# Performance work log

Measured on AMD Instinct MI355X. Metric: run time of the kernel, lower is better.

The kernel has to match this reference:

```python
import jax, jax.numpy as jnp
import numpy as np

N = 100000   # nodes
E = 1200000  # edges
C = 64       # in_channels
H = 64       # hidden_channels
OUT = 10     # out_channels
G = 128      # graphs in batch
L = 3        # num_conv_layers
EPS = 1e-5   # BatchNorm eps


def batchnorm(x, g, b):
    # training-mode BatchNorm1d: biased batch stats over the node/graph axis
    mu = x.mean(axis=0)
    var = x.var(axis=0)
    return (x - mu) * jax.lax.rsqrt(var + EPS) * g + b


def _gcn_norm(edge_index):
    # add self-loops (weight 1) then symmetric normalization deg^-1/2 * w * deg^-1/2
    loop = jnp.arange(N)
    src = jnp.concatenate([edge_index[0], loop])
    dst = jnp.concatenate([edge_index[1], loop])
    w = jnp.ones((E + N,), jnp.float32)
    deg = jax.ops.segment_sum(w, src, num_segments=N)
    dis = jnp.where(deg > 0, jax.lax.rsqrt(deg), 0.0)
    norm = dis[src] * w * dis[dst]
    return src, dst, norm


def gcn_conv(h, W, b, src, dst, norm):
    # linear transform -> gather source features -> edge-normalize -> scatter-add to dst
    hw = h @ W
    msg = norm[:, None] * hw[src]          # [E+N, H]
    return jax.ops.segment_sum(msg, dst, num_segments=N) + b


def setup_inputs() -> dict:
    key = jax.random.key(0)
    ks = jax.random.split(key, 8)
    s = 0.1
    return {
        'x': jax.random.normal(ks[0], (N, C), jnp.float32),
        'edge_index': jax.random.randint(ks[1], (2, E), 0, N),
        'batch_idx': jnp.sort(jax.random.randint(ks[2], (N,), 0, G)),
        # BN params initialized as in the module: weight=1, bias=1e-4
        'bn_feat_g': jnp.ones((C,), jnp.float32),
        'bn_feat_b': jnp.full((C,), 1e-4, jnp.float32),
        'W_feat': jax.random.normal(ks[3], (C, H), jnp.float32) * s,  # conv_feat (gfn=True -> pure linear)
        'b_feat': jnp.zeros((H,), jnp.float32),
        'conv_bn_g': jnp.ones((L, H), jnp.float32),
        'conv_bn_b': jnp.full((L, H), 1e-4, jnp.float32),
        'conv_W': jax.random.normal(ks[4], (L, H, H), jnp.float32) * s,
        'conv_b': jnp.zeros((L, H), jnp.float32),
        'bn_fc_g': jnp.ones((H,), jnp.float32),
        'bn_fc_b': jnp.full((H,), 1e-4, jnp.float32),
        'W_fc': jax.random.normal(ks[5], (H, H), jnp.float32) * s,
        'b_fc': jnp.zeros((H,), jnp.float32),
        'bn_hid_g': jnp.ones((H,), jnp.float32),
        'bn_hid_b': jnp.full((H,), 1e-4, jnp.float32),
        'W_cls': jax.random.normal(ks[6], (H, OUT), jnp.float32) * s,
        'b_cls': jnp.zeros((OUT,), jnp.float32),
    }


def reference(x, edge_index, batch_idx, bn_feat_g, bn_feat_b, W_feat, b_feat,
              conv_bn_g, conv_bn_b, conv_W, conv_b, bn_fc_g, bn_fc_b, W_fc, b_fc,
              bn_hid_g, bn_hid_b, W_cls, b_cls):
    src, dst, norm = _gcn_norm(edge_index)
    # forward_BNConvReLU, residual=False, gating=None, xg=None, dropout=0
    h = batchnorm(x, bn_feat_g, bn_feat_b)
    h = jax.nn.relu(h @ W_feat + b_feat)           # conv_feat: gfn=True => linear only
    for i in range(L):
        h_ = batchnorm(h, conv_bn_g[i], conv_bn_b[i])
        h = jax.nn.relu(gcn_conv(h_, conv_W[i], conv_b[i], src, dst, norm))
    hg = jax.ops.segment_sum(h, batch_idx, num_segments=G)  # global_add_pool -> [G, H]
    h_ = batchnorm(hg, bn_fc_g, bn_fc_b)
    hg = jax.nn.relu(h_ @ W_fc + b_fc)
    hg = batchnorm(hg, bn_hid_g, bn_hid_b)
    logits = hg @ W_cls + b_cls
    return jax.nn.log_softmax(logits, axis=-1)
```

## Files before the change

### kernel.cpp

```cpp
#include <hip/hip_runtime.h>
#include <hip/hip_fp16.h>

#define N_NODES 100000
#define N_EDGES 1200000
#define GRAPHS 128
#define EPSBN 1e-5f


__global__ __launch_bounds__(256) void k_build(const int* __restrict__ src,
                                               const int* __restrict__ dst,
                                               int* __restrict__ cnt,
                                               int* __restrict__ deg,
                                               int* __restrict__ ecsr) {
    int e = blockIdx.x * 256 + threadIdx.x;
    if (e < N_EDGES) {
        int s = src[e], d = dst[e];
        atomicAdd(&deg[s], 1);
        int p = atomicAdd(&cnt[d], 1);
        ecsr[(d << 6) + p] = s;
    }
}

__global__ __launch_bounds__(256) void k_dis(const int* __restrict__ deg,
                                             float* __restrict__ dis) {
    int i = blockIdx.x * 256 + threadIdx.x;
    if (i < N_NODES) dis[i] = rsqrtf((float)deg[i] + 1.0f);
}


__global__ __launch_bounds__(256) void k_sigma(const float* __restrict__ dis,
                                               const int* __restrict__ cnt,
                                               const int* __restrict__ ecsr,
                                               float* __restrict__ sigma) {
    int lane = threadIdx.x & 63;
    int wid = threadIdx.x >> 6;
    for (int node = blockIdx.x * 4 + wid; node < N_NODES; node += gridDim.x * 4) {
        int m = cnt[node];
        float v = 0.f;
        if (lane < m) v = dis[ecsr[(node << 6) + lane]];
#pragma unroll
        for (int d = 1; d <= 32; d <<= 1) v += __shfl_xor(v, d, 64);
        if (lane == 0) {
            float dd = dis[node];
            sigma[node] = dd * (v + dd);
        }
    }
}


__global__ __launch_bounds__(256) void k_stats(const float* __restrict__ x,
                                               float* __restrict__ sums) {
    const float4* x4 = (const float4*)x;
    int t = threadIdx.x;
    int q = t & 15, rg = t >> 4;
    float4 s = {0.f, 0.f, 0.f, 0.f}, s2 = {0.f, 0.f, 0.f, 0.f};
    for (int r = blockIdx.x * 16 + rg; r < N_NODES; r += gridDim.x * 16) {
        float4 v = x4[r * 16 + q];
        s.x += v.x; s.y += v.y; s.z += v.z; s.w += v.w;
        s2.x += v.x * v.x; s2.y += v.y * v.y; s2.z += v.z * v.z; s2.w += v.w * v.w;
    }
    __shared__ float red[2][16][64];
    red[0][rg][q * 4 + 0] = s.x;  red[0][rg][q * 4 + 1] = s.y;
    red[0][rg][q * 4 + 2] = s.z;  red[0][rg][q * 4 + 3] = s.w;
    red[1][rg][q * 4 + 0] = s2.x; red[1][rg][q * 4 + 1] = s2.y;
    red[1][rg][q * 4 + 2] = s2.z; red[1][rg][q * 4 + 3] = s2.w;
    __syncthreads();
    if (t < 64) {
        float a = 0.f, b = 0.f;
#pragma unroll
        for (int k = 0; k < 16; k++) { a += red[0][k][t]; b += red[1][k][t]; }
        atomicAdd(&sums[t], a);
        atomicAdd(&sums[64 + t], b);
    }
}


__global__ __launch_bounds__(256) void k_fold(const float* __restrict__ sums, const float* __restrict__ g,
                       const float* __restrict__ b, const float* __restrict__ W,
                       const float* __restrict__ bias_in, int has_bias,
                       float* __restrict__ Wout, float* __restrict__ bout) {
    __shared__ float a[64], cc[64];
    int t = threadIdx.x;
    if (t < 64) {
        float mu = sums[t] * (1.0f / N_NODES);
        float var = sums[64 + t] * (1.0f / N_NODES) - mu * mu;
        float av = g[t] * rsqrtf(var + EPSBN);
        a[t] = av;
        cc[t] = b[t] - mu * av;
    }
    __syncthreads();
    for (int i = t; i < 4096; i += 256) Wout[i] = a[i >> 6] * W[i];
    if (t < 64) {
        float acc = has_bias ? bias_in[t] : 0.0f;
        for (int k = 0; k < 64; k++) acc += cc[k] * W[k * 64 + t];
        bout[t] = acc;
    }
}


__global__ __launch_bounds__(256, 4) void k_gemm2(const float* __restrict__ X, const float* __restrict__ W,
                        const float* __restrict__ bias, const float* __restrict__ dis,
                        __half* __restrict__ U,
                        float* __restrict__ sums, int do_stats) {
    int t = threadIdx.x;
    int j = t & 63;
    int rg = t >> 6;
    __shared__ float wlds[64][64];
    __shared__ float xs[16][64];
    for (int i = t; i < 4096; i += 256) wlds[i >> 6][i & 63] = W[i];
    float bj = bias[j];
    __syncthreads();
    float s_sum = 0.f, s_sq = 0.f;
    for (int base = blockIdx.x * 16; base < N_NODES; base += gridDim.x * 16) {
        ((float4*)xs)[t] = ((const float4*)(X + base * 64))[t];
        int r0 = rg * 4;
        float a0 = bj, a1 = bj, a2 = bj, a3 = bj;
#pragma unroll
        for (int c = 0; c < 64; c++) {
            float w = wlds[c][j];
            a0 += xs[r0 + 0][c] * w;
            a1 += xs[r0 + 1][c] * w;
            a2 += xs[r0 + 2][c] * w;
            a3 += xs[r0 + 3][c] * w;
        }
        a0 = fmaxf(a0, 0.f); a1 = fmaxf(a1, 0.f);
        a2 = fmaxf(a2, 0.f); a3 = fmaxf(a3, 0.f);
        int nb = base + r0;
        U[(nb + 0) * 64 + j] = __float2half_rn(a0 * dis[nb + 0]);
        U[(nb + 1) * 64 + j] = __float2half_rn(a1 * dis[nb + 1]);
        U[(nb + 2) * 64 + j] = __float2half_rn(a2 * dis[nb + 2]);
        U[(nb + 3) * 64 + j] = __float2half_rn(a3 * dis[nb + 3]);
        if (do_stats) {
            s_sum += a0 + a1 + a2 + a3;
            s_sq += a0 * a0 + a1 * a1 + a2 * a2 + a3 * a3;
        }
    }
    if (do_stats) {
        __syncthreads();
        xs[rg][j] = s_sum;
        xs[4 + rg][j] = s_sq;
        __syncthreads();
        if (t < 64) {
            atomicAdd(&sums[t], xs[0][t] + xs[1][t] + xs[2][t] + xs[3][t]);
            atomicAdd(&sums[64 + t], xs[4][t] + xs[5][t] + xs[6][t] + xs[7][t]);
        }
    }
}


__global__ __launch_bounds__(256, 4) void k_aggemm(const __half* __restrict__ u,
                        const float* __restrict__ dis, const float* __restrict__ sigma,
                        const int* __restrict__ cnt, const int* __restrict__ ecsr,
                        const float* __restrict__ sums_in, const float* __restrict__ bng,
                        const float* __restrict__ bnb,
                        const float* __restrict__ W, const float* __restrict__ bias,
                        __half* __restrict__ uout, float* __restrict__ hout, int last,
                        float* __restrict__ sums_out, int do_stats) {
    const __half2* u2 = (const __half2*)u;
    int t = threadIdx.x;
    int j = t & 63;
    int wid = t >> 6;
    int g = j >> 5, c = j & 31;
    __shared__ float wlds[64][64];
    __shared__ float xs[16][64];
    if (t < 64) {
        float mu = sums_in[t] * (1.0f / N_NODES);
        float var = sums_in[64 + t] * (1.0f / N_NODES) - mu * mu;
        float av = bng[t] * rsqrtf(var + EPSBN);
        xs[0][t] = av;
        xs[1][t] = bnb[t] - mu * av;
    }
    __syncthreads();
    for (int i = t; i < 4096; i += 256) wlds[i >> 6][i & 63] = W[i] * xs[0][i >> 6];
    float cb = 0.f;
#pragma unroll 8
    for (int q = 0; q < 64; q++) cb += xs[1][q] * W[q * 64 + j];
    float bj = bias[j];
    __syncthreads();
    float s_sum = 0.f, s_sq = 0.f;
    for (int base = blockIdx.x * 16; base < N_NODES; base += gridDim.x * 16) {
        int r0 = wid * 4;
        float dvals[4], svals[4];
        for (int r = 0; r < 4; r++) {
            int node = base + r0 + r;
            int m = cnt[node];
            dvals[r] = dis[node];
            svals[r] = sigma[node];
            int sL = 0;
            if (j < m) sL = ecsr[(node << 6) + j];
            float ax = 0.f, ay = 0.f;
#pragma unroll
            for (int k = 0; k < 8; k++) {
                int e = 2 * k + g;
                int sE = __shfl(sL, e, 64);
                float w = (e < m) ? 1.0f : 0.0f;
                float2 f = __half22float2(u2[sE * 32 + c]);
                ax += w * f.x; ay += w * f.y;
            }
            if (m > 16) {
                for (int e = 16 + g; e < m; e += 2) {
                    int sE = __shfl(sL, e, 64);
                    float2 f = __half22float2(u2[sE * 32 + c]);
                    ax += f.x; ay += f.y;
                }
            }
            ax += __shfl_xor(ax, 32, 64);
            ay += __shfl_xor(ay, 32, 64);
            if (g == 0) {
                float2 sf = __half22float2(u2[node * 32 + c]);
                float dd = dvals[r];
                xs[r0 + r][2 * c + 0] = dd * (ax + sf.x);
                xs[r0 + r][2 * c + 1] = dd * (ay + sf.y);
            }
        }
        float a0 = bj + svals[0] * cb, a1 = bj + svals[1] * cb;
        float a2 = bj + svals[2] * cb, a3 = bj + svals[3] * cb;
#pragma unroll
        for (int q = 0; q < 64; q++) {
            float w = wlds[q][j];
            a0 += xs[r0 + 0][q] * w;
            a1 += xs[r0 + 1][q] * w;
            a2 += xs[r0 + 2][q] * w;
            a3 += xs[r0 + 3][q] * w;
        }
        a0 = fmaxf(a0, 0.f); a1 = fmaxf(a1, 0.f);
        a2 = fmaxf(a2, 0.f); a3 = fmaxf(a3, 0.f);
        int nb = base + r0;
        if (last) {
            hout[(nb + 0) * 64 + j] = a0;
            hout[(nb + 1) * 64 + j] = a1;
            hout[(nb + 2) * 64 + j] = a2;
            hout[(nb + 3) * 64 + j] = a3;
        } else {
            uout[(nb + 0) * 64 + j] = __float2half_rn(a0 * dvals[0]);
            uout[(nb + 1) * 64 + j] = __float2half_rn(a1 * dvals[1]);
            uout[(nb + 2) * 64 + j] = __float2half_rn(a2 * dvals[2]);
            uout[(nb + 3) * 64 + j] = __float2half_rn(a3 * dvals[3]);
        }
        if (do_stats) {
            s_sum += a0 + a1 + a2 + a3;
            s_sq += a0 * a0 + a1 * a1 + a2 * a2 + a3 * a3;
        }
    }
    if (do_stats) {
        __syncthreads();
        xs[wid][j] = s_sum;
        xs[4 + wid][j] = s_sq;
        __syncthreads();
        if (t < 64) {
            atomicAdd(&sums_out[t], xs[0][t] + xs[1][t] + xs[2][t] + xs[3][t]);
            atomicAdd(&sums_out[64 + t], xs[4][t] + xs[5][t] + xs[6][t] + xs[7][t]);
        }
    }
}


__global__ __launch_bounds__(256) void k_pool(const float* __restrict__ h, const int* __restrict__ batch,
                       float* __restrict__ hg, float* __restrict__ sums) {
    int g = blockIdx.x;
    int lo = 0, hi = N_NODES;
    while (lo < hi) { int m = (lo + hi) >> 1; if (batch[m] < g) lo = m + 1; else hi = m; }
    int start = lo;
    lo = start; hi = N_NODES;
    while (lo < hi) { int m = (lo + hi) >> 1; if (batch[m] < g + 1) lo = m + 1; else hi = m; }
    int end = lo;
    int c = threadIdx.x & 63, rg = threadIdx.x >> 6;
    float s = 0.f;
    for (int r = start + rg; r < end; r += 4) s += h[r * 64 + c];
    __shared__ float ls[4][64];
    ls[rg][c] = s;
    __syncthreads();
    if (rg == 0) {
        float v = ls[0][c] + ls[1][c] + ls[2][c] + ls[3][c];
        hg[g * 64 + c] = v;
        atomicAdd(&sums[c], v);
        atomicAdd(&sums[64 + c], v * v);
    }
}


__global__ __launch_bounds__(512) void k_tail(const float* __restrict__ hg_in, const float* __restrict__ sums,
                       const float* __restrict__ g1, const float* __restrict__ b1,
                       const float* __restrict__ Wfc, const float* __restrict__ bfc,
                       const float* __restrict__ g2, const float* __restrict__ b2,
                       const float* __restrict__ Wcls, const float* __restrict__ bcls,
                       float* __restrict__ out) {
    __shared__ float hgn[8192];
    __shared__ float h2[8192];
    __shared__ float red[2][8][64];
    __shared__ float a[64], cc[64];
    __shared__ float Wc[640];
    __shared__ float logits[1280];
    __shared__ float lse[128];
    int t = threadIdx.x;
    int j = t & 63;
    int w = t >> 6;

    if (t < 64) {
        float mu = sums[t] * (1.f / 128.f);
        float var = sums[64 + t] * (1.f / 128.f) - mu * mu;
        float av = g1[t] * rsqrtf(var + EPSBN);
        a[t] = av; cc[t] = b1[t] - mu * av;
    }
    for (int i = t; i < 640; i += 512) Wc[i] = Wcls[i];
    __syncthreads();
    for (int i = t; i < 8192; i += 512) hgn[i] = hg_in[i] * a[i & 63] + cc[i & 63];

    float wreg[64];
#pragma unroll
    for (int q = 0; q < 64; q++) wreg[q] = Wfc[q * 64 + j];
    float bj = bfc[j];
    __syncthreads();

    float acc[16];
#pragma unroll
    for (int r = 0; r < 16; r++) acc[r] = bj;
    const float4* hgn4 = (const float4*)hgn;
#pragma unroll
    for (int q4 = 0; q4 < 16; q4++) {
#pragma unroll
        for (int r = 0; r < 16; r++) {
            float4 hv = hgn4[(w * 16 + r) * 16 + q4];
            acc[r] += hv.x * wreg[q4 * 4 + 0] + hv.y * wreg[q4 * 4 + 1]
                    + hv.z * wreg[q4 * 4 + 2] + hv.w * wreg[q4 * 4 + 3];
        }
    }
    float s = 0.f, s2 = 0.f;
#pragma unroll
    for (int r = 0; r < 16; r++) {
        float v = fmaxf(acc[r], 0.f);
        h2[(w * 16 + r) * 64 + j] = v;
        s += v; s2 += v * v;
    }
    red[0][w][j] = s; red[1][w][j] = s2;
    __syncthreads();

    if (t < 64) {
        float su = 0.f, sq = 0.f;
#pragma unroll
        for (int k = 0; k < 8; k++) { su += red[0][k][t]; sq += red[1][k][t]; }
        float mu = su * (1.f / 128.f);
        float var = sq * (1.f / 128.f) - mu * mu;
        float av = g2[t] * rsqrtf(var + EPSBN);
        a[t] = av; cc[t] = b2[t] - mu * av;
    }
    __syncthreads();
    for (int i = t; i < 8192; i += 512) h2[i] = h2[i] * a[i & 63] + cc[i & 63];
    __syncthreads();

    for (int idx = t; idx < 1280; idx += 512) {
        int row = idx / 10, o = idx - row * 10;
        float v = bcls[o];
#pragma unroll
        for (int q = 0; q < 64; q++) v += h2[row * 64 + q] * Wc[q * 10 + o];
        logits[idx] = v;
    }
    __syncthreads();
    if (t < 128) {
        float mx = -1e30f;
#pragma unroll
        for (int o = 0; o < 10; o++) mx = fmaxf(mx, logits[t * 10 + o]);
        float se = 0.f;
#pragma unroll
        for (int o = 0; o < 10; o++) se += expf(logits[t * 10 + o] - mx);
        lse[t] = mx + logf(se);
    }
    __syncthreads();
    for (int idx = t; idx < 1280; idx += 512) out[idx] = logits[idx] - lse[idx / 10];
}


extern "C" void kernel_launch(void* const* d_in, const int* in_sizes, int n_in,
                              void* d_out, int out_size, void* d_ws, size_t ws_size,
                              hipStream_t stream) {
    const float* x         = (const float*)d_in[0];
    const int*   ei        = (const int*)  d_in[1];
    const int*   batch     = (const int*)  d_in[2];
    const float* bn_feat_g = (const float*)d_in[3];
    const float* bn_feat_b = (const float*)d_in[4];
    const float* W_feat    = (const float*)d_in[5];
    const float* b_feat    = (const float*)d_in[6];
    const float* conv_bn_g = (const float*)d_in[7];
    const float* conv_bn_b = (const float*)d_in[8];
    const float* conv_W    = (const float*)d_in[9];
    const float* conv_b    = (const float*)d_in[10];
    const float* bn_fc_g   = (const float*)d_in[11];
    const float* bn_fc_b   = (const float*)d_in[12];
    const float* W_fc      = (const float*)d_in[13];
    const float* b_fc      = (const float*)d_in[14];
    const float* bn_hid_g  = (const float*)d_in[15];
    const float* bn_hid_b  = (const float*)d_in[16];
    const float* W_cls     = (const float*)d_in[17];
    const float* b_cls     = (const float*)d_in[18];
    float* out = (float*)d_out;

    float* ws    = (float*)d_ws;
    float* hbuf  = ws;
    __half* u_a  = (__half*)(ws + 6400000);
    __half* u_b  = (__half*)(ws + 9600000);
    float* dis   = ws + 12800000;
    float* sigma = ws + 12900000;
    float* Wt    = ws + 13000000;
    float* bt    = Wt + 4096;
    float* hg    = bt + 64;
    float* sums  = hg + 8192;
    int*   cnt   = (int*)(sums + 640);
    int*   ecsr  = cnt + 100000;
    int*   deg   = (int*)u_b;

    float* sx = sums;
    float* s0 = sums + 128;
    float* s1 = sums + 256;
    float* s2 = sums + 384;
    float* s3 = sums + 512;

    const int* srcp = ei;
    const int* dstp = ei + N_EDGES;

    hipMemsetAsync(sums, 0, (640 + 100000) * sizeof(float), stream);
    hipMemsetAsync(deg, 0, 100000 * sizeof(int), stream);

    k_build<<<(N_EDGES + 255) / 256, 256, 0, stream>>>(srcp, dstp, cnt, deg, ecsr);
    k_dis<<<(N_NODES + 255) / 256, 256, 0, stream>>>(deg, dis);
    k_sigma<<<1024, 256, 0, stream>>>(dis, cnt, ecsr, sigma);

    k_stats<<<512, 256, 0, stream>>>(x, sx);
    k_fold<<<1, 256, 0, stream>>>(sx, bn_feat_g, bn_feat_b, W_feat, b_feat, 1, Wt, bt);
    k_gemm2<<<2048, 256, 0, stream>>>(x, Wt, bt, dis, u_a, s0, 1);

    k_aggemm<<<2048, 256, 0, stream>>>(u_a, dis, sigma, cnt, ecsr,
                                       s0, conv_bn_g + 0, conv_bn_b + 0,
                                       conv_W + 0, conv_b + 0,
                                       u_b, nullptr, 0, s1, 1);
    k_aggemm<<<2048, 256, 0, stream>>>(u_b, dis, sigma, cnt, ecsr,
                                       s1, conv_bn_g + 64, conv_bn_b + 64,
                                       conv_W + 4096, conv_b + 64,
                                       u_a, nullptr, 0, s2, 1);
    k_aggemm<<<2048, 256, 0, stream>>>(u_a, dis, sigma, cnt, ecsr,
                                       s2, conv_bn_g + 128, conv_bn_b + 128,
                                       conv_W + 8192, conv_b + 128,
                                       nullptr, hbuf, 1, nullptr, 0);

    k_pool<<<GRAPHS, 256, 0, stream>>>(hbuf, batch, hg, s3);
    k_tail<<<1, 512, 0, stream>>>(hg, s3, bn_fc_g, bn_fc_b, W_fc, b_fc,
                                  bn_hid_g, bn_hid_b, W_cls, b_cls, out);
}
```

Before: 629.0 us.

## Split pooling across more blocks, vectorize LDS matmuls, hoist per-node loads

Global pooling now runs four blocks per graph that each atomically add a quarter-range partial into a zeroed hg buffer. The graph-level BN statistics move into the tail kernel. The LDS matmul inner loops in k_gemm2 and k_aggemm now read float4 rows, and k_aggemm loads the per-node cnt/ecsr/dis/sigma/self features for all four rows up front to expose memory-level parallelism. k_sigma issues its loads unconditionally. Extra register pressure and atomics on hg are the trade-offs.

```diff
diff --git a/kernel.cpp b/kernel.cpp
--- a/kernel.cpp
+++ b/kernel.cpp
@@ -36,14 +36,13 @@
     int wid = threadIdx.x >> 6;
     for (int node = blockIdx.x * 4 + wid; node < N_NODES; node += gridDim.x * 4) {
         int m = cnt[node];
-        float v = 0.f;
-        if (lane < m) v = dis[ecsr[(node << 6) + lane]];
+        int sraw = ecsr[(node << 6) + lane];
+        float dd = dis[node];
+        int sL = (lane < m) ? sraw : 0;
+        float v = (lane < m) ? dis[sL] : 0.f;
 #pragma unroll
         for (int d = 1; d <= 32; d <<= 1) v += __shfl_xor(v, d, 64);
-        if (lane == 0) {
-            float dd = dis[node];
-            sigma[node] = dd * (v + dd);
-        }
+        if (lane == 0) sigma[node] = dd * (v + dd);
     }
 }
 
@@ -115,13 +114,18 @@
         ((float4*)xs)[t] = ((const float4*)(X + base * 64))[t];
         int r0 = rg * 4;
         float a0 = bj, a1 = bj, a2 = bj, a3 = bj;
-#pragma unroll
-        for (int c = 0; c < 64; c++) {
-            float w = wlds[c][j];
-            a0 += xs[r0 + 0][c] * w;
-            a1 += xs[r0 + 1][c] * w;
-            a2 += xs[r0 + 2][c] * w;
-            a3 += xs[r0 + 3][c] * w;
+        const float4* x0 = (const float4*)xs[r0 + 0];
+        const float4* x1 = (const float4*)xs[r0 + 1];
+        const float4* x2 = (const float4*)xs[r0 + 2];
+        const float4* x3 = (const float4*)xs[r0 + 3];
+#pragma unroll
+        for (int q4 = 0; q4 < 16; q4++) {
+            float w0 = wlds[q4 * 4 + 0][j], w1 = wlds[q4 * 4 + 1][j];
+            float w2 = wlds[q4 * 4 + 2][j], w3 = wlds[q4 * 4 + 3][j];
+            float4 v0 = x0[q4]; a0 += v0.x * w0 + v0.y * w1 + v0.z * w2 + v0.w * w3;
+            float4 v1 = x1[q4]; a1 += v1.x * w0 + v1.y * w1 + v1.z * w2 + v1.w * w3;
+            float4 v2 = x2[q4]; a2 += v2.x * w0 + v2.y * w1 + v2.z * w2 + v2.w * w3;
+            float4 v3 = x3[q4]; a3 += v3.x * w0 + v3.y * w1 + v3.z * w2 + v3.w * w3;
         }
         a0 = fmaxf(a0, 0.f); a1 = fmaxf(a1, 0.f);
         a2 = fmaxf(a2, 0.f); a3 = fmaxf(a3, 0.f);
@@ -180,14 +184,22 @@
     float s_sum = 0.f, s_sq = 0.f;
     for (int base = blockIdx.x * 16; base < N_NODES; base += gridDim.x * 16) {
         int r0 = wid * 4;
+        int nb = base + r0;
+        int mm[4], srw[4];
         float dvals[4], svals[4];
+        __half2 selfs[4];
+#pragma unroll
         for (int r = 0; r < 4; r++) {
-            int node = base + r0 + r;
-            int m = cnt[node];
-            dvals[r] = dis[node];
-            svals[r] = sigma[node];
-            int sL = 0;
-            if (j < m) sL = ecsr[(node << 6) + j];
+            mm[r] = cnt[nb + r];
+            srw[r] = ecsr[((nb + r) << 6) + j];
+            dvals[r] = dis[nb + r];
+            svals[r] = sigma[nb + r];
+            selfs[r] = u2[(nb + r) * 32 + c];
+        }
+#pragma unroll
+        for (int r = 0; r < 4; r++) {
+            int m = mm[r];
+            int sL = (j < m) ? srw[r] : 0;
             float ax = 0.f, ay = 0.f;
 #pragma unroll
             for (int k = 0; k < 8; k++) {
@@ -207,7 +219,7 @@
             ax += __shfl_xor(ax, 32, 64);
             ay += __shfl_xor(ay, 32, 64);
             if (g == 0) {
-                float2 sf = __half22float2(u2[node * 32 + c]);
+                float2 sf = __half22float2(selfs[r]);
                 float dd = dvals[r];
                 xs[r0 + r][2 * c + 0] = dd * (ax + sf.x);
                 xs[r0 + r][2 * c + 1] = dd * (ay + sf.y);
@@ -215,17 +227,21 @@
         }
         float a0 = bj + svals[0] * cb, a1 = bj + svals[1] * cb;
         float a2 = bj + svals[2] * cb, a3 = bj + svals[3] * cb;
-#pragma unroll
-        for (int q = 0; q < 64; q++) {
-            float w = wlds[q][j];
-            a0 += xs[r0 + 0][q] * w;
-            a1 += xs[r0 + 1][q] * w;
-            a2 += xs[r0 + 2][q] * w;
-            a3 += xs[r0 + 3][q] * w;
+        const float4* x0 = (const float4*)xs[r0 + 0];
+        const float4* x1 = (const float4*)xs[r0 + 1];
+        const float4* x2 = (const float4*)xs[r0 + 2];
+        const float4* x3 = (const float4*)xs[r0 + 3];
+#pragma unroll
+        for (int q4 = 0; q4 < 16; q4++) {
+            float w0 = wlds[q4 * 4 + 0][j], w1 = wlds[q4 * 4 + 1][j];
+            float w2 = wlds[q4 * 4 + 2][j], w3 = wlds[q4 * 4 + 3][j];
+            float4 v0 = x0[q4]; a0 += v0.x * w0 + v0.y * w1 + v0.z * w2 + v0.w * w3;
+            float4 v1 = x1[q4]; a1 += v1.x * w0 + v1.y * w1 + v1.z * w2 + v1.w * w3;
+            float4 v2 = x2[q4]; a2 += v2.x * w0 + v2.y * w1 + v2.z * w2 + v2.w * w3;
+            float4 v3 = x3[q4]; a3 += v3.x * w0 + v3.y * w1 + v3.z * w2 + v3.w * w3;
         }
         a0 = fmaxf(a0, 0.f); a1 = fmaxf(a1, 0.f);
         a2 = fmaxf(a2, 0.f); a3 = fmaxf(a3, 0.f);
-        int nb = base + r0;
         if (last) {
             hout[(nb + 0) * 64 + j] = a0;
             hout[(nb + 1) * 64 + j] = a1;
@@ -256,30 +272,28 @@
 
 
 __global__ __launch_bounds__(256) void k_pool(const float* __restrict__ h, const int* __restrict__ batch,
-                       float* __restrict__ hg, float* __restrict__ sums) {
-    int g = blockIdx.x;
+                       float* __restrict__ hg) {
+    int g = blockIdx.x >> 2, q3 = blockIdx.x & 3;
     int lo = 0, hi = N_NODES;
     while (lo < hi) { int m = (lo + hi) >> 1; if (batch[m] < g) lo = m + 1; else hi = m; }
     int start = lo;
     lo = start; hi = N_NODES;
     while (lo < hi) { int m = (lo + hi) >> 1; if (batch[m] < g + 1) lo = m + 1; else hi = m; }
     int end = lo;
+    int len = end - start;
+    int c0 = start + ((len * q3) >> 2);
+    int c1 = start + ((len * (q3 + 1)) >> 2);
     int c = threadIdx.x & 63, rg = threadIdx.x >> 6;
     float s = 0.f;
-    for (int r = start + rg; r < end; r += 4) s += h[r * 64 + c];
+    for (int r = c0 + rg; r < c1; r += 4) s += h[r * 64 + c];
     __shared__ float ls[4][64];
     ls[rg][c] = s;
     __syncthreads();
-    if (rg == 0) {
-        float v = ls[0][c] + ls[1][c] + ls[2][c] + ls[3][c];
-        hg[g * 64 + c] = v;
-        atomicAdd(&sums[c], v);
-        atomicAdd(&sums[64 + c], v * v);
-    }
-}
-
-
-__global__ __launch_bounds__(512) void k_tail(const float* __restrict__ hg_in, const float* __restrict__ sums,
+    if (rg == 0) atomicAdd(&hg[g * 64 + c], ls[0][c] + ls[1][c] + ls[2][c] + ls[3][c]);
+}
+
+
+__global__ __launch_bounds__(512) void k_tail(const float* __restrict__ hg_in,
                        const float* __restrict__ g1, const float* __restrict__ b1,
                        const float* __restrict__ Wfc, const float* __restrict__ bfc,
                        const float* __restrict__ g2, const float* __restrict__ b2,
@@ -296,13 +310,26 @@
     int j = t & 63;
     int w = t >> 6;
 
-    if (t < 64) {
-        float mu = sums[t] * (1.f / 128.f);
-        float var = sums[64 + t] * (1.f / 128.f) - mu * mu;
+    {
+        float su = 0.f, sq = 0.f;
+#pragma unroll
+        for (int gg = 0; gg < 16; gg++) {
+            float v = hg_in[(w * 16 + gg) * 64 + j];
+            su += v; sq += v * v;
+        }
+        red[0][w][j] = su; red[1][w][j] = sq;
+    }
+    for (int i = t; i < 640; i += 512) Wc[i] = Wcls[i];
+    __syncthreads();
+    if (t < 64) {
+        float su = 0.f, sq = 0.f;
+#pragma unroll
+        for (int k = 0; k < 8; k++) { su += red[0][k][t]; sq += red[1][k][t]; }
+        float mu = su * (1.f / 128.f);
+        float var = sq * (1.f / 128.f) - mu * mu;
         float av = g1[t] * rsqrtf(var + EPSBN);
         a[t] = av; cc[t] = b1[t] - mu * av;
     }
-    for (int i = t; i < 640; i += 512) Wc[i] = Wcls[i];
     __syncthreads();
     for (int i = t; i < 8192; i += 512) hgn[i] = hg_in[i] * a[i & 63] + cc[i & 63];
 
@@ -412,12 +439,11 @@
     float* s0 = sums + 128;
     float* s1 = sums + 256;
     float* s2 = sums + 384;
-    float* s3 = sums + 512;
 
     const int* srcp = ei;
     const int* dstp = ei + N_EDGES;
 
-    hipMemsetAsync(sums, 0, (640 + 100000) * sizeof(float), stream);
+    hipMemsetAsync(hg, 0, (8192 + 640 + 100000) * sizeof(float), stream);
     hipMemsetAsync(deg, 0, 100000 * sizeof(int), stream);
 
     k_build<<<(N_EDGES + 255) / 256, 256, 0, stream>>>(srcp, dstp, cnt, deg, ecsr);
@@ -441,7 +467,7 @@
                                        conv_W + 8192, conv_b + 128,
                                        nullptr, hbuf, 1, nullptr, 0);
 
-    k_pool<<<GRAPHS, 256, 0, stream>>>(hbuf, batch, hg, s3);
-    k_tail<<<1, 512, 0, stream>>>(hg, s3, bn_fc_g, bn_fc_b, W_fc, b_fc,
+    k_pool<<<4 * GRAPHS, 256, 0, stream>>>(hbuf, batch, hg);
+    k_tail<<<1, 512, 0, stream>>>(hg, bn_fc_g, bn_fc_b, W_fc, b_fc,
                                   bn_hid_g, bn_hid_b, W_cls, b_cls, out);
 }
```

Result: faster. 552.4 us (-12.2%).
